# Optimization experiments

Hardware: AMD Instinct MI355X
Metric: run time of the kernel (lower is better)

## Reference

```python
import jax, jax.numpy as jnp
import numpy as np

B, T, IN, H, OUT = 64, 512, 256, 1024, 1


def _uniform(key, shape, k):
    return jax.random.uniform(key, shape, jnp.float32, -k, k)


def setup_inputs() -> dict:
    key = jax.random.key(0)
    ks = jax.random.split(key, 12)
    k = 1.0 / np.sqrt(H)
    return {
        "x": jax.random.normal(ks[0], (B, T, IN), jnp.float32),
        "W_ih0": _uniform(ks[1], (3 * H, IN), k),
        "W_hh0": _uniform(ks[2], (3 * H, H), k),
        "b_ih0": _uniform(ks[3], (3 * H,), k),
        "b_hh0": _uniform(ks[4], (3 * H,), k),
        "W_ih1": _uniform(ks[5], (3 * H, H), k),
        "W_hh1": _uniform(ks[6], (3 * H, H), k),
        "b_ih1": _uniform(ks[7], (3 * H,), k),
        "b_hh1": _uniform(ks[8], (3 * H,), k),
        "W_fc": _uniform(ks[9], (OUT, H), 1.0 / np.sqrt(H)),
        "b_fc": _uniform(ks[10], (OUT,), 1.0 / np.sqrt(H)),
    }


def _gru_layer(x, W_ih, W_hh, b_ih, b_hh):
    # x: [B, T, D_in] -> outputs [B, T, H], final hidden [B, H]
    # Precompute input projections for all timesteps (one big GEMM).
    xg = jnp.einsum('btd,gd->btg', x, W_ih) + b_ih  # [B, T, 3H]
    xg = jnp.swapaxes(xg, 0, 1)  # [T, B, 3H]

    def step(h, xg_t):
        hg = h @ W_hh.T + b_hh  # [B, 3H]
        xr, xz, xn = jnp.split(xg_t, 3, axis=-1)
        hr, hz, hn = jnp.split(hg, 3, axis=-1)
        r = jax.nn.sigmoid(xr + hr)
        z = jax.nn.sigmoid(xz + hz)
        n = jnp.tanh(xn + r * hn)
        h_new = (1.0 - z) * n + z * h
        return h_new, h_new

    h0 = jnp.zeros((x.shape[0], W_hh.shape[1]), x.dtype)
    h_final, ys = jax.lax.scan(step, h0, xg)
    return jnp.swapaxes(ys, 0, 1), h_final


def reference(x, W_ih0, W_hh0, b_ih0, b_hh0, W_ih1, W_hh1, b_ih1, b_hh1, W_fc, b_fc):
    # Inference mode: dropout (between GRU layers and before fc) is identity.
    y0, _ = _gru_layer(x, W_ih0, W_hh0, b_ih0, b_hh0)
    _, h_last = _gru_layer(y0, W_ih1, W_hh1, b_ih1, b_hh1)
    return h_last @ W_fc.T + b_fc  # [B, OUT]
```

## Files before the change

### kernel.cpp

```cpp
#include <hip/hip_runtime.h>
#include <hip/hip_bf16.h>
#include <stdint.h>


constexpr int TSEQ = 512;
constexpr int NB   = 64;
constexpr int HD   = 1024;
constexpr int IND  = 256;
constexpr int NWG  = 256;
constexpr int FS   = 16;
constexpr int PL   = NB * HD;

typedef float f32x4  __attribute__((ext_vector_type(4)));
typedef short short8 __attribute__((ext_vector_type(8)));

__device__ __forceinline__ float bf2f(unsigned u) {
    return __builtin_bit_cast(float, u << 16);
}
__device__ __forceinline__ unsigned short f2bf(float f) {
    unsigned u = __builtin_bit_cast(unsigned, f);
    u += 0x7fffu + ((u >> 16) & 1u);
    return (unsigned short)(u >> 16);
}
__device__ __forceinline__ float sigm(float x) { return 1.0f / (1.0f + __expf(-x)); }
__device__ __forceinline__ float tanh_fast(float x) { return 1.0f - 2.0f / (1.0f + __expf(2.0f * x)); }

__device__ __forceinline__ void cstore16(unsigned short* p, unsigned short v) {
    __hip_atomic_store(p, v, __ATOMIC_RELAXED, __HIP_MEMORY_SCOPE_AGENT);
}
__device__ __forceinline__ unsigned short cload16(const unsigned short* p) {
    return __hip_atomic_load(p, __ATOMIC_RELAXED, __HIP_MEMORY_SCOPE_AGENT);
}

#define MFMA(a, b, c) __builtin_amdgcn_mfma_f32_16x16x32_bf16((a), (b), (c), 0, 0, 0)

#define LDA16(dst, base, imm) \
    asm volatile("global_load_dwordx4 %0, %1, off offset:%2 sc0 sc1" \
                 : "=v"(dst) : "v"(base), "i"(imm))
#define LDX16(dst, base, imm) \
    asm volatile("global_load_dwordx4 %0, %1, off offset:%2" \
                 : "=v"(dst) : "v"(base), "i"(imm))
#define VWAIT(n) do { asm volatile("s_waitcnt vmcnt(" #n ")" ::: "memory"); \
                      __builtin_amdgcn_sched_barrier(0); } while (0)

__global__ void convert_w(const float* __restrict__ src, unsigned short* __restrict__ dst, int n) {
    int i = blockIdx.x * blockDim.x + threadIdx.x;
    int stride = gridDim.x * blockDim.x;
    for (; i < n; i += stride) dst[i] = f2bf(src[i]);
}

__global__ __launch_bounds__(512, 2) void gru_main(
    const float* __restrict__ x,
    const unsigned short* __restrict__ wih0,
    const unsigned short* __restrict__ whh0,
    const unsigned short* __restrict__ wih1,
    const unsigned short* __restrict__ whh1,
    const float* __restrict__ bih0, const float* __restrict__ bhh0,
    const float* __restrict__ bih1, const float* __restrict__ bhh1,
    const float* __restrict__ wfc,  const float* __restrict__ bfc,
    unsigned short* __restrict__ h0hi, unsigned short* __restrict__ h0lo,
    unsigned short* __restrict__ h1hi, unsigned short* __restrict__ h1lo,
    int* __restrict__ arrive,
    float* __restrict__ out)
{
    const int wg    = blockIdx.x;
    const int layer = wg >> 7;
    const int cc    = wg & 127;
    const int jb8   = cc << 3;
    const int tid   = threadIdx.x;
    const int wid   = tid >> 6;
    const int kh    = wid >> 2;
    const int mw    = wid & 3;
    const int lane  = tid & 63;
    const int l15   = lane & 15;
    const int c8    = l15 & 7;
    const int kg8   = (lane >> 4) << 3;
    const int arow  = (mw << 4) + l15;
    const int kb    = kh << 9;
    const int ckb   = kh << 4;
    const int kbx   = kh << 7;

    const unsigned short* Whh = layer ? whh1 : whh0;
    const unsigned short* Wih = layer ? wih1 : wih0;
    const float* bih = layer ? bih1 : bih0;
    const float* bhh = layer ? bhh1 : bhh0;
    unsigned short* hhi = layer ? h1hi : h0hi;
    unsigned short* hlo = layer ? h1lo : h0lo;

    const int jg = jb8 + c8;

    const float bias_r  = bih[jg]        + bhh[jg];
    const float bias_z  = bih[HD + jg]   + bhh[HD + jg];
    const float bias_nx = bih[2*HD + jg];
    const float bias_nh = bhh[2*HD + jg];

    __shared__ unsigned short wlds[192 * 256];
    __shared__ float part[16 * 4 * 64];
    __shared__ float red[256];

    if (layer == 1) {
        #pragma unroll
        for (int i = 0; i < 12; ++i) {
            int f = tid + i * 512;
            int s   = f >> 10;
            int rem = f & 1023;
            int ck  = rem >> 5;
            int hi  = (rem >> 3) & 3;
            int c   = rem & 7;
            const unsigned short* src = (s < 3 ? Whh : Wih)
                + (size_t)((s % 3) * HD + jb8 + c) * HD + ck * 32 + hi * 8;
            *(short8*)(wlds + (s * 32 + ck) * 256 + hi * 64 + c * 8) =
                *(const short8*)src;
        }
    } else {
        #pragma unroll
        for (int i = 0; i < 6; ++i) {
            int f = tid + i * 512;
            int s   = f >> 10;
            int rem = f & 1023;
            int ck  = rem >> 5;
            int hi  = (rem >> 3) & 3;
            int c   = rem & 7;
            const unsigned short* src = Whh
                + (size_t)(s * HD + jb8 + c) * HD + ck * 32 + hi * 8;
            *(short8*)(wlds + (s * 32 + ck) * 256 + hi * 64 + c * 8) =
                *(const short8*)src;
        }
        for (int i = 0; i < 2; ++i) {
            int f = tid + i * 512;
            if (f < 768) {
                int s   = f >> 8;
                int rem = f & 255;
                int ck  = rem >> 5;
                int hi  = (rem >> 3) & 3;
                int c   = rem & 7;
                const unsigned short* src = Wih
                    + (size_t)(s * HD + jb8 + c) * IND + ck * 32 + hi * 8;
                *(short8*)(wlds + (96 + s * 8 + ck) * 256 + hi * 64 + c * 8) =
                    *(const short8*)src;
            }
        }
    }
    __syncthreads();

    const int lws = (lane >> 4) * 64 + c8 * 8;
#define LW(blk) (*(const short8*)(wlds + (blk) * 256 + lws))

    float hold[4] = {0.f, 0.f, 0.f, 0.f};

    for (int iter = 0; iter <= TSEQ; ++iter) {
        const bool active = layer ? (iter >= 1) : (iter < TSEQ);
        if (active) {
            const int t     = layer ? (iter - 1) : iter;
            const int rs    = (t + 1) & 1;
            const int wslot = t & 1;
            const unsigned short* hrhi = hhi + rs * PL;
            const unsigned short* hrlo = hlo + rs * PL;
            const unsigned short* bAh = hrhi + (size_t)arow * HD + kb + kg8;
            const unsigned short* bAl = hrlo + (size_t)arow * HD + kb + kg8;

            f32x4 ar  = {0.f, 0.f, 0.f, 0.f};
            f32x4 az  = {0.f, 0.f, 0.f, 0.f};
            f32x4 ahn = {0.f, 0.f, 0.f, 0.f};
            f32x4 axn = {0.f, 0.f, 0.f, 0.f};

            if (layer == 0) {
                const float* px = x + ((size_t)arow * TSEQ + t) * IND + kbx + kg8;
                short8 Ah[5], Al[5], Wa[3], Wb[3];
#define L0A(c) do { LDA16(Ah[(c)%5], bAh, (c)*64); LDA16(Al[(c)%5], bAl, (c)*64); } while (0)
#define L0X(c) do { LDX16(Ah[(c)%5], px, ((c)-16)*128); LDX16(Al[(c)%5], px, ((c)-16)*128+16); } while (0)
#define WR0(c, WB) do { WB[0] = LW(ckb + (c)); WB[1] = LW(32 + ckb + (c)); \
                        WB[2] = LW(64 + ckb + (c)); } while (0)
#define WX0(c, WB) do { int xck = (ckb >> 2) + (c) - 16; \
                        WB[0] = LW(96 + xck); WB[1] = LW(104 + xck); \
                        WB[2] = LW(112 + xck); } while (0)
#define MR0(c, WB) do { \
    ar  = MFMA(Ah[(c)%5], WB[0], ar);  ar  = MFMA(Al[(c)%5], WB[0], ar);  \
    az  = MFMA(Ah[(c)%5], WB[1], az);  az  = MFMA(Al[(c)%5], WB[1], az);  \
    ahn = MFMA(Ah[(c)%5], WB[2], ahn); ahn = MFMA(Al[(c)%5], WB[2], ahn); } while (0)
#define MX0(c, WB) do { \
    float4 xa = __builtin_bit_cast(float4, Ah[(c)%5]); \
    float4 xc = __builtin_bit_cast(float4, Al[(c)%5]); \
    short8 af; \
    af[0] = (short)f2bf(xa.x); af[1] = (short)f2bf(xa.y); \
    af[2] = (short)f2bf(xa.z); af[3] = (short)f2bf(xa.w); \
    af[4] = (short)f2bf(xc.x); af[5] = (short)f2bf(xc.y); \
    af[6] = (short)f2bf(xc.z); af[7] = (short)f2bf(xc.w); \
    ar  = MFMA(af, WB[0], ar); \
    az  = MFMA(af, WB[1], az); \
    axn = MFMA(af, WB[2], axn); } while (0)
                WR0(0, Wa);
                L0A(0); L0A(1); L0A(2); L0A(3);
                WR0(1,  Wb); L0A(4);  VWAIT(8); MR0(0,  Wa);
                WR0(2,  Wa); L0A(5);  VWAIT(8); MR0(1,  Wb);
                WR0(3,  Wb); L0A(6);  VWAIT(8); MR0(2,  Wa);
                WR0(4,  Wa); L0A(7);  VWAIT(8); MR0(3,  Wb);
                WR0(5,  Wb); L0A(8);  VWAIT(8); MR0(4,  Wa);
                WR0(6,  Wa); L0A(9);  VWAIT(8); MR0(5,  Wb);
                WR0(7,  Wb); L0A(10); VWAIT(8); MR0(6,  Wa);
                WR0(8,  Wa); L0A(11); VWAIT(8); MR0(7,  Wb);
                WR0(9,  Wb); L0A(12); VWAIT(8); MR0(8,  Wa);
                WR0(10, Wa); L0A(13); VWAIT(8); MR0(9,  Wb);
                WR0(11, Wb); L0A(14); VWAIT(8); MR0(10, Wa);
                WR0(12, Wa); L0A(15); VWAIT(8); MR0(11, Wb);
                WR0(13, Wb); L0X(16); VWAIT(8); MR0(12, Wa);
                WR0(14, Wa); L0X(17); VWAIT(8); MR0(13, Wb);
                WR0(15, Wb); L0X(18); VWAIT(8); MR0(14, Wa);
                WX0(16, Wa); L0X(19); VWAIT(8); MR0(15, Wb);
                WX0(17, Wb); VWAIT(6); MX0(16, Wa);
                WX0(18, Wa); VWAIT(4); MX0(17, Wb);
                WX0(19, Wb); VWAIT(2); MX0(18, Wa);
                             VWAIT(0); MX0(19, Wb);
            } else {
                const unsigned short* bAy = h0hi + (size_t)wslot * PL
                                                 + (size_t)arow * HD + kb + kg8;
                short8 Ah[5], Al[5], Ay[5], Wa[6], Wb[6];
#define L1A(c) do { LDA16(Ah[(c)%5], bAh, (c)*64); LDA16(Al[(c)%5], bAl, (c)*64); \
                    LDA16(Ay[(c)%5], bAy, (c)*64); } while (0)
#define WR1(c, WB) do { WB[0] = LW(ckb + (c)); WB[1] = LW(32 + ckb + (c)); \
    WB[2] = LW(64 + ckb + (c)); WB[3] = LW(96 + ckb + (c)); \
    WB[4] = LW(128 + ckb + (c)); WB[5] = LW(160 + ckb + (c)); } while (0)
#define MF1(c, WB) do { \
    ar  = MFMA(Ah[(c)%5], WB[0], ar);  ar  = MFMA(Al[(c)%5], WB[0], ar);  \
    ar  = MFMA(Ay[(c)%5], WB[3], ar); \
    az  = MFMA(Ah[(c)%5], WB[1], az);  az  = MFMA(Al[(c)%5], WB[1], az);  \
    az  = MFMA(Ay[(c)%5], WB[4], az); \
    ahn = MFMA(Ah[(c)%5], WB[2], ahn); ahn = MFMA(Al[(c)%5], WB[2], ahn); \
    axn = MFMA(Ay[(c)%5], WB[5], axn); } while (0)
                WR1(0, Wa);
                L1A(0); L1A(1); L1A(2); L1A(3);
                WR1(1,  Wb); L1A(4);  VWAIT(12); MF1(0,  Wa);
                WR1(2,  Wa); L1A(5);  VWAIT(12); MF1(1,  Wb);
                WR1(3,  Wb); L1A(6);  VWAIT(12); MF1(2,  Wa);
                WR1(4,  Wa); L1A(7);  VWAIT(12); MF1(3,  Wb);
                WR1(5,  Wb); L1A(8);  VWAIT(12); MF1(4,  Wa);
                WR1(6,  Wa); L1A(9);  VWAIT(12); MF1(5,  Wb);
                WR1(7,  Wb); L1A(10); VWAIT(12); MF1(6,  Wa);
                WR1(8,  Wa); L1A(11); VWAIT(12); MF1(7,  Wb);
                WR1(9,  Wb); L1A(12); VWAIT(12); MF1(8,  Wa);
                WR1(10, Wa); L1A(13); VWAIT(12); MF1(9,  Wb);
                WR1(11, Wb); L1A(14); VWAIT(12); MF1(10, Wa);
                WR1(12, Wa); L1A(15); VWAIT(12); MF1(11, Wb);
                WR1(13, Wb); VWAIT(9); MF1(12, Wa);
                WR1(14, Wa); VWAIT(6); MF1(13, Wb);
                WR1(15, Wb); VWAIT(3); MF1(14, Wa);
                             VWAIT(0); MF1(15, Wb);
            }

            if (kh) {
                #pragma unroll
                for (int e = 0; e < 4; ++e) {
                    part[((0*4 + e) * 4 + mw) * 64 + lane] = ar[e];
                    part[((1*4 + e) * 4 + mw) * 64 + lane] = az[e];
                    part[((2*4 + e) * 4 + mw) * 64 + lane] = ahn[e];
                    part[((3*4 + e) * 4 + mw) * 64 + lane] = axn[e];
                }
            }
            __syncthreads();
            if (!kh) {
                unsigned short* hwhi = hhi + wslot * PL;
                unsigned short* hwlo = hlo + wslot * PL;
                #pragma unroll
                for (int e = 0; e < 4; ++e) {
                    const float arr = ar[e]  + part[((0*4 + e) * 4 + mw) * 64 + lane];
                    const float azz = az[e]  + part[((1*4 + e) * 4 + mw) * 64 + lane];
                    const float ahh = ahn[e] + part[((2*4 + e) * 4 + mw) * 64 + lane];
                    const float axx = axn[e] + part[((3*4 + e) * 4 + mw) * 64 + lane];
                    const int bat = (mw << 4) + ((lane >> 4) << 2) + e;
                    const size_t idx = (size_t)bat * HD + jg;
                    float r = sigm(arr + bias_r);
                    float z = sigm(azz + bias_z);
                    float n = tanh_fast(axx + bias_nx + r * (ahh + bias_nh));
                    float hnew = (1.0f - z) * n + z * hold[e];
                    hold[e] = hnew;
                    if (l15 < 8) {
                        unsigned short hi_ = f2bf(hnew);
                        cstore16(hwhi + idx, hi_);
                        cstore16(hwlo + idx, f2bf(hnew - bf2f((unsigned)hi_)));
                    }
                }
            }
        }

        asm volatile("s_waitcnt vmcnt(0)" ::: "memory");
        __syncthreads();
        if (tid == 0) {
            atomicAdd(&arrive[(size_t)iter * FS], 1);
            int spins = 0;
            while (__hip_atomic_load(&arrive[(size_t)iter * FS],
                                     __ATOMIC_RELAXED, __HIP_MEMORY_SCOPE_AGENT) < NWG) {
                __builtin_amdgcn_s_sleep(1);
                if (++spins > (1 << 20)) break;
            }
        }
        __syncthreads();
    }

    if (wg == 0) {
        const int fslot = (TSEQ - 1) & 1;
        const unsigned short* hf_hi = h1hi + (size_t)fslot * PL;
        const unsigned short* hf_lo = h1lo + (size_t)fslot * PL;
        if (tid < 256) {
            const int bat  = tid & 63;
            const int pidx = tid >> 6;
            const int k0   = pidx * (HD / 4);
            float s = 0.0f;
            for (int k = 0; k < HD / 4; ++k) {
                size_t idx = (size_t)bat * HD + k0 + k;
                s += (bf2f((unsigned)cload16(hf_hi + idx)) +
                      bf2f((unsigned)cload16(hf_lo + idx))) * wfc[k0 + k];
            }
            red[tid] = s;
        }
        __syncthreads();
        if (tid < 64)
            out[tid] = red[tid] + red[tid + 64] + red[tid + 128] + red[tid + 192] + bfc[0];
    }
}

extern "C" void kernel_launch(void* const* d_in, const int* in_sizes, int n_in,
                              void* d_out, int out_size, void* d_ws, size_t ws_size,
                              hipStream_t stream) {
    const float* x    = (const float*)d_in[0];
    const float* Wih0 = (const float*)d_in[1];
    const float* Whh0 = (const float*)d_in[2];
    const float* bih0 = (const float*)d_in[3];
    const float* bhh0 = (const float*)d_in[4];
    const float* Wih1 = (const float*)d_in[5];
    const float* Whh1 = (const float*)d_in[6];
    const float* bih1 = (const float*)d_in[7];
    const float* bhh1 = (const float*)d_in[8];
    const float* Wfc  = (const float*)d_in[9];
    const float* bfc  = (const float*)d_in[10];
    float* out = (float*)d_out;

    char* ws = (char*)d_ws;
    size_t off = 0;
    int* arrive = (int*)(ws + off);               off += (size_t)(TSEQ + 1) * FS * 4;
    unsigned short* h0hi = (unsigned short*)(ws + off); off += (size_t)2 * PL * 2;
    unsigned short* h0lo = (unsigned short*)(ws + off); off += (size_t)2 * PL * 2;
    unsigned short* h1hi = (unsigned short*)(ws + off); off += (size_t)2 * PL * 2;
    unsigned short* h1lo = (unsigned short*)(ws + off); off += (size_t)2 * PL * 2;
    size_t zero_bytes = off;
    unsigned short* wih0b = (unsigned short*)(ws + off); off += (size_t)3 * HD * IND * 2;
    unsigned short* whh0b = (unsigned short*)(ws + off); off += (size_t)3 * HD * HD * 2;
    unsigned short* wih1b = (unsigned short*)(ws + off); off += (size_t)3 * HD * HD * 2;
    unsigned short* whh1b = (unsigned short*)(ws + off); off += (size_t)3 * HD * HD * 2;
    if (off > ws_size) return;

    hipMemsetAsync(d_ws, 0, zero_bytes, stream);
    hipMemsetAsync(d_out, 0, (size_t)out_size * sizeof(float), stream);

    convert_w<<<512, 256, 0, stream>>>(Wih0, wih0b, 3 * HD * IND);
    convert_w<<<512, 256, 0, stream>>>(Whh0, whh0b, 3 * HD * HD);
    convert_w<<<512, 256, 0, stream>>>(Wih1, wih1b, 3 * HD * HD);
    convert_w<<<512, 256, 0, stream>>>(Whh1, whh1b, 3 * HD * HD);

    gru_main<<<NWG, 512, 0, stream>>>(x, wih0b, whh0b, wih1b, whh1b,
                                      bih0, bhh0, bih1, bhh1, Wfc, bfc,
                                      h0hi, h0lo, h1hi, h1lo, arrive, out);
}
```

Measured before the change: 8.586 ms.

## Stage hidden state into per-XCD copies before each timestep's GEMM

Each timestep, the workgroups on the same XCD now cooperatively copy the four hidden-state planes (with cache-bypassing loads) into a per-XCD staging buffer. After that copy they synchronise through a per-XCD arrival counter. The main MFMA loads then read the staged copy with sc0 only, so they can hit the XCD-local L2 instead of bypassing to memory. This adds an extra copy pass, a per-XCD barrier every step and a startup registration spin, in exchange for cheaper repeated hidden-state reads.

New measurement: 9.869 ms. 14.9% more time.

```diff
diff --git a/kernel.cpp b/kernel.cpp
--- a/kernel.cpp
+++ b/kernel.cpp
@@ -10,6 +10,7 @@
 constexpr int NWG  = 256;
 constexpr int FS   = 16;
 constexpr int PL   = NB * HD;
+constexpr int CHT  = 4 * PL / 8;
 
 typedef float f32x4  __attribute__((ext_vector_type(4)));
 typedef short short8 __attribute__((ext_vector_type(8)));
@@ -34,8 +35,10 @@
 
 #define MFMA(a, b, c) __builtin_amdgcn_mfma_f32_16x16x32_bf16((a), (b), (c), 0, 0, 0)
 
-#define LDA16(dst, base, imm) \
-    asm volatile("global_load_dwordx4 %0, %1, off offset:%2 sc0 sc1" \
+#define LDC16(dst, ptr) \
+    asm volatile("global_load_dwordx4 %0, %1, off sc0 sc1" : "=v"(dst) : "v"(ptr))
+#define LDB16(dst, base, imm) \
+    asm volatile("global_load_dwordx4 %0, %1, off offset:%2 sc0" \
                  : "=v"(dst) : "v"(base), "i"(imm))
 #define LDX16(dst, base, imm) \
     asm volatile("global_load_dwordx4 %0, %1, off offset:%2" \
@@ -60,7 +63,9 @@
     const float* __restrict__ wfc,  const float* __restrict__ bfc,
     unsigned short* __restrict__ h0hi, unsigned short* __restrict__ h0lo,
     unsigned short* __restrict__ h1hi, unsigned short* __restrict__ h1lo,
-    int* __restrict__ arrive,
+    unsigned short* __restrict__ stg,
+    int* __restrict__ larr, int* __restrict__ arrive,
+    int* __restrict__ xcnt, int* __restrict__ regcnt,
     float* __restrict__ out)
 {
     const int wg    = blockIdx.x;
@@ -97,6 +102,7 @@
     __shared__ unsigned short wlds[192 * 256];
     __shared__ float part[16 * 4 * 64];
     __shared__ float red[256];
+    __shared__ int sh_rank, sh_ng;
 
     if (layer == 1) {
         #pragma unroll
@@ -141,7 +147,38 @@
             }
         }
     }
+
+    unsigned xcd;
+    asm("s_getreg_b32 %0, hwreg(HW_REG_XCC_ID)" : "=s"(xcd));
+    xcd &= 7;
+    unsigned short* stx = stg + (size_t)xcd * 4 * PL;
+    if (tid == 0) {
+        sh_rank = __hip_atomic_fetch_add(&xcnt[xcd * FS], 1,
+                                         __ATOMIC_RELAXED, __HIP_MEMORY_SCOPE_AGENT);
+        __hip_atomic_fetch_add(regcnt, 1, __ATOMIC_RELAXED, __HIP_MEMORY_SCOPE_AGENT);
+        int spins = 0;
+        while (__hip_atomic_load(regcnt, __ATOMIC_RELAXED,
+                                 __HIP_MEMORY_SCOPE_AGENT) < NWG) {
+            __builtin_amdgcn_s_sleep(1);
+            if (++spins > (1 << 20)) break;
+        }
+        sh_ng = __hip_atomic_load(&xcnt[xcd * FS], __ATOMIC_RELAXED,
+                                  __HIP_MEMORY_SCOPE_AGENT);
+    }
     __syncthreads();
+    const int rank = sh_rank;
+    const int ng   = sh_ng;
+    const int slice = (CHT + ng - 1) / ng;
+
+    const unsigned short *bAh, *bAl, *bAy = nullptr;
+    if (layer == 0) {
+        bAh = stx + 0 * PL + (size_t)arow * HD + kb + kg8;
+        bAl = stx + 1 * PL + (size_t)arow * HD + kb + kg8;
+    } else {
+        bAh = stx + 2 * PL + (size_t)arow * HD + kb + kg8;
+        bAl = stx + 3 * PL + (size_t)arow * HD + kb + kg8;
+        bAy = stx + 0 * PL + (size_t)arow * HD + kb + kg8;
+    }
 
     const int lws = (lane >> 4) * 64 + c8 * 8;
 #define LW(blk) (*(const short8*)(wlds + (blk) * 256 + lws))
@@ -149,15 +186,44 @@
     float hold[4] = {0.f, 0.f, 0.f, 0.f};
 
     for (int iter = 0; iter <= TSEQ; ++iter) {
+        {
+            const unsigned short* c0 = h0hi + ((iter + 1) & 1) * PL;
+            const unsigned short* c1 = h0lo + ((iter + 1) & 1) * PL;
+            const unsigned short* c2 = h1hi + (iter & 1) * PL;
+            const unsigned short* c3 = h1lo + (iter & 1) * PL;
+            const int p0 = rank * slice;
+            const int p1 = (p0 + slice < CHT) ? (p0 + slice) : CHT;
+            for (int base = p0; base < p1; base += 512) {
+                int f = base + tid;
+                f = (f < p1) ? f : (p1 - 1);
+                const int pl = f >> 13;
+                const int q  = f & 8191;
+                const unsigned short* s =
+                    (pl == 0) ? c0 : (pl == 1) ? c1 : (pl == 2) ? c2 : c3;
+                short8 v;
+                LDC16(v, s + (size_t)q * 8);
+                VWAIT(0);
+                *(short8*)(stx + (size_t)pl * PL + (size_t)q * 8) = v;
+            }
+        }
+        asm volatile("s_waitcnt vmcnt(0)" ::: "memory");
+        __syncthreads();
+        if (tid == 0) {
+            int* lp = larr + ((size_t)iter * 8 + xcd) * FS;
+            atomicAdd(lp, 1);
+            int spins = 0;
+            while (__hip_atomic_load(lp, __ATOMIC_RELAXED,
+                                     __HIP_MEMORY_SCOPE_AGENT) < ng) {
+                __builtin_amdgcn_s_sleep(1);
+                if (++spins > (1 << 20)) break;
+            }
+        }
+        __syncthreads();
+
         const bool active = layer ? (iter >= 1) : (iter < TSEQ);
         if (active) {
             const int t     = layer ? (iter - 1) : iter;
-            const int rs    = (t + 1) & 1;
             const int wslot = t & 1;
-            const unsigned short* hrhi = hhi + rs * PL;
-            const unsigned short* hrlo = hlo + rs * PL;
-            const unsigned short* bAh = hrhi + (size_t)arow * HD + kb + kg8;
-            const unsigned short* bAl = hrlo + (size_t)arow * HD + kb + kg8;
 
             f32x4 ar  = {0.f, 0.f, 0.f, 0.f};
             f32x4 az  = {0.f, 0.f, 0.f, 0.f};
@@ -167,7 +233,7 @@
             if (layer == 0) {
                 const float* px = x + ((size_t)arow * TSEQ + t) * IND + kbx + kg8;
                 short8 Ah[5], Al[5], Wa[3], Wb[3];
-#define L0A(c) do { LDA16(Ah[(c)%5], bAh, (c)*64); LDA16(Al[(c)%5], bAl, (c)*64); } while (0)
+#define L0A(c) do { LDB16(Ah[(c)%5], bAh, (c)*64); LDB16(Al[(c)%5], bAl, (c)*64); } while (0)
 #define L0X(c) do { LDX16(Ah[(c)%5], px, ((c)-16)*128); LDX16(Al[(c)%5], px, ((c)-16)*128+16); } while (0)
 #define WR0(c, WB) do { WB[0] = LW(ckb + (c)); WB[1] = LW(32 + ckb + (c)); \
                         WB[2] = LW(64 + ckb + (c)); } while (0)
@@ -212,11 +278,9 @@
                 WX0(19, Wb); VWAIT(2); MX0(18, Wa);
                              VWAIT(0); MX0(19, Wb);
             } else {
-                const unsigned short* bAy = h0hi + (size_t)wslot * PL
-                                                 + (size_t)arow * HD + kb + kg8;
                 short8 Ah[5], Al[5], Ay[5], Wa[6], Wb[6];
-#define L1A(c) do { LDA16(Ah[(c)%5], bAh, (c)*64); LDA16(Al[(c)%5], bAl, (c)*64); \
-                    LDA16(Ay[(c)%5], bAy, (c)*64); } while (0)
+#define L1A(c) do { LDB16(Ah[(c)%5], bAh, (c)*64); LDB16(Al[(c)%5], bAl, (c)*64); \
+                    LDB16(Ay[(c)%5], bAy, (c)*64); } while (0)
 #define WR1(c, WB) do { WB[0] = LW(ckb + (c)); WB[1] = LW(32 + ckb + (c)); \
     WB[2] = LW(64 + ckb + (c)); WB[3] = LW(96 + ckb + (c)); \
     WB[4] = LW(128 + ckb + (c)); WB[5] = LW(160 + ckb + (c)); } while (0)
@@ -336,12 +400,16 @@
 
     char* ws = (char*)d_ws;
     size_t off = 0;
-    int* arrive = (int*)(ws + off);               off += (size_t)(TSEQ + 1) * FS * 4;
+    int* arrive = (int*)(ws + off); off += (size_t)(TSEQ + 1) * FS * 4;
+    int* larr   = (int*)(ws + off); off += (size_t)(TSEQ + 1) * 8 * FS * 4;
+    int* xcnt   = (int*)(ws + off); off += (size_t)8 * FS * 4;
+    int* regcnt = (int*)(ws + off); off += (size_t)FS * 4;
     unsigned short* h0hi = (unsigned short*)(ws + off); off += (size_t)2 * PL * 2;
     unsigned short* h0lo = (unsigned short*)(ws + off); off += (size_t)2 * PL * 2;
     unsigned short* h1hi = (unsigned short*)(ws + off); off += (size_t)2 * PL * 2;
     unsigned short* h1lo = (unsigned short*)(ws + off); off += (size_t)2 * PL * 2;
     size_t zero_bytes = off;
+    unsigned short* stg = (unsigned short*)(ws + off); off += (size_t)8 * 4 * PL * 2;
     unsigned short* wih0b = (unsigned short*)(ws + off); off += (size_t)3 * HD * IND * 2;
     unsigned short* whh0b = (unsigned short*)(ws + off); off += (size_t)3 * HD * HD * 2;
     unsigned short* wih1b = (unsigned short*)(ws + off); off += (size_t)3 * HD * HD * 2;
@@ -358,5 +426,6 @@
 
     gru_main<<<NWG, 512, 0, stream>>>(x, wih0b, whh0b, wih1b, whh1b,
                                       bih0, bhh0, bih1, bhh1, Wfc, bfc,
-                                      h0hi, h0lo, h1hi, h1lo, arrive, out);
-}
+                                      h0hi, h0lo, h1hi, h1lo, stg,
+                                      larr, arrive, xcnt, regcnt, out);
+}
```

## Replace flat grid barrier with two-level tree barrier and per-group release flags

Applied to the files above, without the earlier changes.

The single global arrival counter, which all 256 workgroups atomically increment and then poll, is replaced by a hierarchical barrier. Workgroups first arrive on a counter shared by a group of 8. The last arrival of each group increments a top-level counter, and the final arriver writes 32 release flags, each on its own padded line. Each workgroup then polls only its group's flag, which is meant to cut atomic contention and polling traffic on one cache line. The cost is extra latency from two atomic hops plus 32 serial release stores, and the sleep interval rises from 1 to 2.

After: 7.108 ms. 1.21x faster.

```diff
diff --git a/kernel.cpp b/kernel.cpp
--- a/kernel.cpp
+++ b/kernel.cpp
@@ -60,7 +60,7 @@
     const float* __restrict__ wfc,  const float* __restrict__ bfc,
     unsigned short* __restrict__ h0hi, unsigned short* __restrict__ h0lo,
     unsigned short* __restrict__ h1hi, unsigned short* __restrict__ h1lo,
-    int* __restrict__ arrive,
+    int* __restrict__ lvl0, int* __restrict__ lvl1, int* __restrict__ rel,
     float* __restrict__ out)
 {
     const int wg    = blockIdx.x;
@@ -285,11 +285,27 @@
         asm volatile("s_waitcnt vmcnt(0)" ::: "memory");
         __syncthreads();
         if (tid == 0) {
-            atomicAdd(&arrive[(size_t)iter * FS], 1);
+            const int g = wg >> 3;
+            int* l0p = lvl0 + ((size_t)iter * 32 + g) * FS;
+            int old = __hip_atomic_fetch_add(l0p, 1, __ATOMIC_RELAXED,
+                                             __HIP_MEMORY_SCOPE_AGENT);
+            if (old == 7) {
+                int old2 = __hip_atomic_fetch_add(lvl1 + (size_t)iter * FS, 1,
+                                                  __ATOMIC_RELAXED,
+                                                  __HIP_MEMORY_SCOPE_AGENT);
+                if (old2 == 31) {
+                    #pragma unroll
+                    for (int k = 0; k < 32; ++k)
+                        __hip_atomic_store(rel + ((size_t)iter * 32 + k) * FS, 1,
+                                           __ATOMIC_RELAXED,
+                                           __HIP_MEMORY_SCOPE_AGENT);
+                }
+            }
+            int* rp = rel + ((size_t)iter * 32 + g) * FS;
             int spins = 0;
-            while (__hip_atomic_load(&arrive[(size_t)iter * FS],
-                                     __ATOMIC_RELAXED, __HIP_MEMORY_SCOPE_AGENT) < NWG) {
-                __builtin_amdgcn_s_sleep(1);
+            while (__hip_atomic_load(rp, __ATOMIC_RELAXED,
+                                     __HIP_MEMORY_SCOPE_AGENT) < 1) {
+                __builtin_amdgcn_s_sleep(2);
                 if (++spins > (1 << 20)) break;
             }
         }
@@ -336,7 +352,9 @@
 
     char* ws = (char*)d_ws;
     size_t off = 0;
-    int* arrive = (int*)(ws + off);               off += (size_t)(TSEQ + 1) * FS * 4;
+    int* lvl0 = (int*)(ws + off); off += (size_t)(TSEQ + 1) * 32 * FS * 4;
+    int* lvl1 = (int*)(ws + off); off += (size_t)(TSEQ + 1) * FS * 4;
+    int* rel  = (int*)(ws + off); off += (size_t)(TSEQ + 1) * 32 * FS * 4;
     unsigned short* h0hi = (unsigned short*)(ws + off); off += (size_t)2 * PL * 2;
     unsigned short* h0lo = (unsigned short*)(ws + off); off += (size_t)2 * PL * 2;
     unsigned short* h1hi = (unsigned short*)(ws + off); off += (size_t)2 * PL * 2;
@@ -358,5 +376,6 @@
 
     gru_main<<<NWG, 512, 0, stream>>>(x, wih0b, whh0b, wih1b, whh1b,
                                       bih0, bhh0, bih1, bhh1, Wfc, bfc,
-                                      h0hi, h0lo, h1hi, h1lo, arrive, out);
-}
+                                      h0hi, h0lo, h1hi, h1lo,
+                                      lvl0, lvl1, rel, out);
+}
```
